# Kernel optimization log

Measured on AMD Instinct MI355X. Metric: run time of the kernel, lower is better.

The kernel has to match this reference:

```python
import jax, jax.numpy as jnp
import numpy as np
import math

B, S, D, H = 8, 1024, 1024, 16
DK = D          # d_k = d_v = d_model (required for the per-head matmul to type-check)
HD = DK // H    # per-head dim = 64


def setup_inputs() -> dict:
    key = jax.random.key(0)
    ks = jax.random.split(key, 10)
    sc = 0.02
    return {
        "source": jax.random.normal(ks[0], (B, S, D), dtype=jnp.float32),
        "target": jax.random.normal(ks[1], (B, S, D), dtype=jnp.float32),
        "wq": jax.random.normal(ks[2], (D, DK), dtype=jnp.float32) * sc,
        "wk": jax.random.normal(ks[3], (D, DK), dtype=jnp.float32) * sc,
        "wv": jax.random.normal(ks[4], (D, DK), dtype=jnp.float32) * sc,
        "WQ": jax.random.normal(ks[5], (H, D, HD), dtype=jnp.float32) * sc,
        "WK": jax.random.normal(ks[6], (H, D, HD), dtype=jnp.float32) * sc,
        "WV": jax.random.normal(ks[7], (H, D, HD), dtype=jnp.float32) * sc,
        "ow": jax.random.normal(ks[8], (DK, D), dtype=jnp.float32) * sc,
        "ob": jnp.zeros((D,), dtype=jnp.float32),
    }


def reference(source, target, wq, wk, wv, WQ, WK, WV, ow, ob):
    # shared projections (nn.Linear, bias=False)
    Q = source @ wq          # (B,S,DK)
    K = target @ wk          # (B,S,DK)
    V = target @ wv          # (B,S,DK)
    # per-head projections Q @ W_Q[i], vectorized over all heads
    q = jnp.einsum('bsk,hkd->bhsd', Q, WQ)   # (B,H,S,HD)
    k = jnp.einsum('bsk,hkd->bhsd', K, WK)
    v = jnp.einsum('bsk,hkd->bhsd', V, WV)
    scores = jnp.einsum('bhqd,bhkd->bhqk', q, k) / math.sqrt(DK)
    # NOTE: original uses nn.Softmax(dim=1) on (B, Sq, Sk) -> normalizes over
    # the QUERY axis; faithful translation => axis=2 of (B,H,Sq,Sk).
    attn = jax.nn.softmax(scores, axis=2)
    o = jnp.einsum('bhqk,bhkd->bhqd', attn, v)          # (B,H,S,HD)
    o = jnp.transpose(o, (0, 2, 1, 3)).reshape(B, S, DK)  # concat heads
    return o @ ow + ob
```

## Files before the change

kernel.cpp:

```cpp
#include <hip/hip_runtime.h>

using u16 = unsigned short;
typedef float f32x4 __attribute__((ext_vector_type(4)));
typedef __bf16 bf16x8 __attribute__((ext_vector_type(8)));
typedef unsigned short u16x4 __attribute__((ext_vector_type(4)));
typedef unsigned short u16x8 __attribute__((ext_vector_type(8)));
typedef unsigned int u32x2 __attribute__((ext_vector_type(2)));

static constexpr float SC2 = 0.03125f * 1.44269504088896f;

static __device__ __forceinline__ u16 f2bf(float f) {
  unsigned u = __builtin_bit_cast(unsigned, f);
  u += 0x7FFFu + ((u >> 16) & 1u);
  return (u16)(u >> 16);
}
static __device__ __forceinline__ float bf2f(u16 h) {
  unsigned u = ((unsigned)h) << 16;
  return __builtin_bit_cast(float, u);
}
static __device__ __forceinline__ unsigned cvt_pk(float lo, float hi) {
  unsigned r;
  asm("v_cvt_pk_bf16_f32 %0, %1, %2" : "=v"(r) : "v"(lo), "v"(hi));
  return r;
}

typedef __attribute__((address_space(3))) unsigned int lds_uint;
typedef __attribute__((address_space(1))) unsigned int g_uint;

static __device__ __forceinline__ void load_lds16(const u16* gp, const void* lp) {
  __builtin_amdgcn_global_load_lds((g_uint*)(unsigned long long)gp,
                                   (lds_uint*)(unsigned int)(unsigned long long)lp,
                                   16, 0, 0);
}

struct Prep {
  const float* src; const float* tgt;
  const float* w[3]; const float* W[3]; const float* ow;
  u16* src_bf; u16* tgt_bf; u16* w_bf[3]; u16* Wt[3]; u16* owT;
};
__global__ __launch_bounds__(256) void k_prep(Prep P) {
  const int bid = blockIdx.x, t = threadIdx.x;
  if (bid < 16384) {
    const float* in = bid < 8192 ? P.src : P.tgt;
    u16* out = bid < 8192 ? P.src_bf : P.tgt_bf;
    int i = (bid & 8191) * 256 + t;
    f32x4 v = reinterpret_cast<const f32x4*>(in)[i];
    u16x4 o;
    o[0] = f2bf(v[0]); o[1] = f2bf(v[1]); o[2] = f2bf(v[2]); o[3] = f2bf(v[3]);
    reinterpret_cast<u16x4*>(out)[i] = o;
  } else if (bid < 19456) {
    int r = bid - 16384;
    int z = r >> 10;
    int i = (r & 1023) * 256 + t;
    f32x4 v = reinterpret_cast<const f32x4*>(P.w[z])[i];
    u16x4 o;
    o[0] = f2bf(v[0]); o[1] = f2bf(v[1]); o[2] = f2bf(v[2]); o[3] = f2bf(v[3]);
    reinterpret_cast<u16x4*>(P.w_bf[z])[i] = o;
  } else if (bid < 31744) {
    int r = bid - 19456;
    int z = r >> 12;
    int idx = (r & 4095) * 256 + t;
    int n = idx >> 10, c = idx & 1023;
    int h = n >> 6, j = n & 63;
    P.Wt[z][idx] = f2bf(P.W[z][(h * 1024 + c) * 64 + j]);
  } else {
    int idx = (bid - 31744) * 256 + t;
    int n = idx >> 10, k = idx & 1023;
    P.owT[idx] = f2bf(P.ow[k * 1024 + n]);
  }
}

struct GemmPtrs { const u16* A; const u16* B; void* C; float scale; int mode; };
struct Gemm3 { GemmPtrs g[3]; };

__global__ __launch_bounds__(256) void k_gemm_bt(Gemm3 P, int N, int K,
                                                 const float* __restrict__ bias) {
  const u16* A  = P.g[blockIdx.z].A;
  const u16* Bt = P.g[blockIdx.z].B;
  const float sc = P.g[blockIdx.z].scale;
  const int mode = P.g[blockIdx.z].mode;
  __shared__ u16 As[2][128 * 64];
  __shared__ u16 Bs[2][128 * 64];
  const int tid = threadIdx.x, lane = tid & 63, w = tid >> 6;
  const int swz = (blockIdx.x & 7) * (gridDim.x >> 3) + (blockIdx.x >> 3);
  const int nbn = N >> 7;
  const int m0 = (swz / nbn) << 7;
  const int n0 = (swz % nbn) << 7;
  const int wr = (w >> 1) << 6, wc = (w & 1) << 6;
  const int l15 = lane & 15, lg = lane >> 4;
  const int srow = tid >> 3;
  const int sslot = (tid & 7) ^ (srow & 7);
  const u16* Ag = A  + (size_t)(m0 + srow) * K + sslot * 8;
  const u16* Bg = Bt + (size_t)(n0 + srow) * K + sslot * 8;

  f32x4 acc[4][4];
#pragma unroll
  for (int i = 0; i < 4; ++i)
#pragma unroll
    for (int j = 0; j < 4; ++j) acc[i][j] = f32x4{0.f, 0.f, 0.f, 0.f};

#pragma unroll
  for (int j = 0; j < 4; ++j) {
    load_lds16(Ag + (size_t)(j * 32) * K, (const char*)As[0] + j * 4096 + tid * 16);
    load_lds16(Bg + (size_t)(j * 32) * K, (const char*)Bs[0] + j * 4096 + tid * 16);
  }
  __syncthreads();

  for (int kt = 0; kt < K; kt += 64) {
    const int buf = (kt >> 6) & 1;
    if (kt + 64 < K) {
#pragma unroll
      for (int j = 0; j < 4; ++j) {
        load_lds16(Ag + (size_t)(j * 32) * K + kt + 64, (const char*)As[buf ^ 1] + j * 4096 + tid * 16);
        load_lds16(Bg + (size_t)(j * 32) * K + kt + 64, (const char*)Bs[buf ^ 1] + j * 4096 + tid * 16);
      }
    }
#pragma unroll
    for (int kh = 0; kh < 2; ++kh) {
      bf16x8 af[4], bfr[4];
#pragma unroll
      for (int i = 0; i < 4; ++i) {
        const int ra = wr + i * 16 + l15;
        const int rb = wc + i * 16 + l15;
        af[i]  = *reinterpret_cast<const bf16x8*>(As[buf] + ra * 64 + ((((kh << 2) | lg) ^ (ra & 7)) << 3));
        bfr[i] = *reinterpret_cast<const bf16x8*>(Bs[buf] + rb * 64 + ((((kh << 2) | lg) ^ (rb & 7)) << 3));
      }
#pragma unroll
      for (int mi = 0; mi < 4; ++mi)
#pragma unroll
        for (int ni = 0; ni < 4; ++ni)
          acc[mi][ni] = __builtin_amdgcn_mfma_f32_16x16x32_bf16(af[mi], bfr[ni], acc[mi][ni], 0, 0, 0);
    }
    __syncthreads();
  }

  const int orow0 = m0 + wr + lg * 4;
  const int ocol0 = n0 + wc + l15;
  if (mode == 1) {
    float* C = (float*)P.g[blockIdx.z].C;
#pragma unroll
    for (int ni = 0; ni < 4; ++ni) {
      float bv = bias ? bias[ocol0 + ni * 16] : 0.f;
#pragma unroll
      for (int mi = 0; mi < 4; ++mi)
#pragma unroll
        for (int r = 0; r < 4; ++r)
          C[(size_t)(orow0 + mi * 16 + r) * N + ocol0 + ni * 16] = acc[mi][ni][r] + bv;
    }
  } else if (mode == 2) {
    u16* C = (u16*)P.g[blockIdx.z].C;
    const int b = m0 >> 10;
    const int kk0 = (orow0 & 1023);
#pragma unroll
    for (int ni = 0; ni < 4; ++ni) {
      const int col = ocol0 + ni * 16;
      const int hh = col >> 6, d = col & 63;
      u16* vbase = C + ((size_t)(b * 16 + hh)) * 65536 + d * 1024 + kk0;
#pragma unroll
      for (int mi = 0; mi < 4; ++mi) {
        u16x4 pv;
#pragma unroll
        for (int r = 0; r < 4; ++r) pv[r] = f2bf(acc[mi][ni][r] * sc);
        *reinterpret_cast<u16x4*>(vbase + mi * 16) = pv;
      }
    }
  } else {
    u16* C = (u16*)P.g[blockIdx.z].C;
#pragma unroll
    for (int ni = 0; ni < 4; ++ni)
#pragma unroll
      for (int mi = 0; mi < 4; ++mi)
#pragma unroll
        for (int r = 0; r < 4; ++r)
          C[(size_t)(orow0 + mi * 16 + r) * N + ocol0 + ni * 16] = f2bf(acc[mi][ni][r] * sc);
  }
}

__global__ __launch_bounds__(256) void k_pass1(const u16* __restrict__ q_all,
                                               const u16* __restrict__ k_all,
                                               float* __restrict__ l_buf) {
  const int bh = blockIdx.x, kb = blockIdx.y;
  const int b = bh >> 4, h = bh & 15;
  __shared__ u16 Qs[2][2048];
  const int t = threadIdx.x;
  const int lane = t & 63, w = t >> 6;
  const int l15 = lane & 15, lg = lane >> 4;
  const u16* qp = q_all + (size_t)b * 1048576 + h * 64;
  const u16* kp = k_all + (size_t)b * 1048576 + h * 64;
  const int kc0 = kb * 128 + w * 32;

  bf16x8 bfr[2][2];
#pragma unroll
  for (int c = 0; c < 2; ++c)
#pragma unroll
    for (int ks = 0; ks < 2; ++ks)
      bfr[c][ks] = *reinterpret_cast<const bf16x8*>(
          kp + (size_t)(kc0 + c * 16 + l15) * 1024 + ks * 32 + lg * 8);

  const int qrow = t >> 3, qslot = (t & 7) ^ (qrow & 7);
  const u16* qg = qp + (size_t)qrow * 1024 + (qslot << 3);

  load_lds16(qg, (const char*)&Qs[0][0] + t * 16);
  __syncthreads();

  float acc0 = 0.f, acc1 = 0.f;
  const int qsw = l15 & 7;

#pragma unroll 1
  for (int qt = 0; qt < 1024; qt += 32) {
    const int buf = (qt >> 5) & 1;
    if (qt + 32 < 1024)
      load_lds16(qg + (size_t)(qt + 32) * 1024, (const char*)&Qs[buf ^ 1][0] + t * 16);
    const u16* Qb = Qs[buf];
    bf16x8 aq[2][2];
#pragma unroll
    for (int qf = 0; qf < 2; ++qf) {
      aq[qf][0] = *reinterpret_cast<const bf16x8*>(Qb + (qf * 16 + l15) * 64 + ((lg ^ qsw) << 3));
      aq[qf][1] = *reinterpret_cast<const bf16x8*>(Qb + (qf * 16 + l15) * 64 + (((4 + lg) ^ qsw) << 3));
    }
#pragma unroll
    for (int qf = 0; qf < 2; ++qf)
#pragma unroll
      for (int c = 0; c < 2; ++c) {
        f32x4 z = {0.f, 0.f, 0.f, 0.f};
        f32x4 s = __builtin_amdgcn_mfma_f32_16x16x32_bf16(aq[qf][0], bfr[c][0], z, 0, 0, 0);
        s = __builtin_amdgcn_mfma_f32_16x16x32_bf16(aq[qf][1], bfr[c][1], s, 0, 0, 0);
        float e = __builtin_amdgcn_exp2f(s[0]) + __builtin_amdgcn_exp2f(s[1])
                + __builtin_amdgcn_exp2f(s[2]) + __builtin_amdgcn_exp2f(s[3]);
        if (c) acc1 += e; else acc0 += e;
      }
    __syncthreads();
  }
  acc0 += __shfl_xor(acc0, 16); acc0 += __shfl_xor(acc0, 32);
  acc1 += __shfl_xor(acc1, 16); acc1 += __shfl_xor(acc1, 32);
  if (lane < 32) {
    int col = kc0 + lane;
    l_buf[(size_t)bh * 1024 + col] = (lane < 16) ? acc0 : acc1;
  }
}

__global__ __launch_bounds__(256, 4) void k_pass2(const u16* __restrict__ q_all,
                                                  const u16* __restrict__ k_all,
                                                  const u16* __restrict__ vT,
                                                  const float* __restrict__ l_buf,
                                                  u16* __restrict__ o_all) {
  const int bh = blockIdx.x, qb = blockIdx.y;
  const int b = bh >> 4, h = bh & 15;
  __shared__ u16 Ks[2][2048];
  __shared__ u16 Vs[2][2048];
  __shared__ u16 p_lds[4][2][640];
  __shared__ float rl_lds[1024];
  const int t = threadIdx.x;
  const int lane = t & 63, w = t >> 6;
  const int l15 = lane & 15, lg = lane >> 4;
  const int q0 = qb * 128 + w * 32;
  const u16* qp = q_all + (size_t)b * 1048576 + h * 64;
  const u16* kp = k_all + (size_t)b * 1048576 + h * 64;
  const u16* vp = vT + (size_t)bh * 65536;

  {
    f32x4 lv = reinterpret_cast<const f32x4*>(l_buf + (size_t)bh * 1024)[t];
    f32x4 rv;
#pragma unroll
    for (int j = 0; j < 4; ++j) rv[j] = 1.0f / lv[j];
    reinterpret_cast<f32x4*>(rl_lds)[t] = rv;
  }

  const int krow = t >> 3, kslot = (t & 7) ^ (krow & 7);
  const u16* kg = kp + (size_t)krow * 1024 + (kslot << 3);
  const int vrow = t >> 2, vslot = (t & 3) ^ (vrow & 3);
  const u16* vg = vp + (size_t)vrow * 1024 + (vslot << 3);

  bf16x8 bq[2][2];
#pragma unroll
  for (int qf = 0; qf < 2; ++qf)
#pragma unroll
    for (int s = 0; s < 2; ++s)
      bq[qf][s] = *reinterpret_cast<const bf16x8*>(
          qp + (size_t)(q0 + qf * 16 + l15) * 1024 + s * 32 + lg * 8);

  f32x4 od[2][4];
#pragma unroll
  for (int qf = 0; qf < 2; ++qf)
#pragma unroll
    for (int n = 0; n < 4; ++n) od[qf][n] = f32x4{0.f, 0.f, 0.f, 0.f};

  load_lds16(kg, (const char*)&Ks[0][0] + t * 16);
  load_lds16(vg, (const char*)&Vs[0][0] + t * 16);
  __syncthreads();

  const int ksw = l15 & 7, vsw = l15 & 3;

#pragma unroll 1
  for (int kt = 0; kt < 1024; kt += 32) {
    const int buf = (kt >> 5) & 1;
    if (kt + 32 < 1024) {
      load_lds16(kg + (size_t)(kt + 32) * 1024, (const char*)&Ks[buf ^ 1][0] + t * 16);
      load_lds16(vg + (kt + 32), (const char*)&Vs[buf ^ 1][0] + t * 16);
    }
    const u16* Kb = Ks[buf];
    const u16* Vb = Vs[buf];
    bf16x8 k00 = *reinterpret_cast<const bf16x8*>(Kb + l15 * 64 + ((lg ^ ksw) << 3));
    bf16x8 k01 = *reinterpret_cast<const bf16x8*>(Kb + l15 * 64 + (((4 + lg) ^ ksw) << 3));
    bf16x8 k10 = *reinterpret_cast<const bf16x8*>(Kb + (16 + l15) * 64 + ((lg ^ ksw) << 3));
    bf16x8 k11 = *reinterpret_cast<const bf16x8*>(Kb + (16 + l15) * 64 + (((4 + lg) ^ ksw) << 3));
    bf16x8 vc[4];
#pragma unroll
    for (int n = 0; n < 4; ++n)
      vc[n] = *reinterpret_cast<const bf16x8*>(Vb + (n * 16 + l15) * 32 + ((lg ^ vsw) << 3));

    f32x4 r0 = *reinterpret_cast<const f32x4*>(&rl_lds[kt + lg * 4]);
    f32x4 r1 = *reinterpret_cast<const f32x4*>(&rl_lds[kt + 16 + lg * 4]);

    u16* pl = p_lds[w][0];
    u16* ph = p_lds[w][1];
#pragma unroll
    for (int qf = 0; qf < 2; ++qf) {
      f32x4 z = {0.f, 0.f, 0.f, 0.f};
      f32x4 s0 = __builtin_amdgcn_mfma_f32_16x16x32_bf16(k00, bq[qf][0], z, 0, 0, 0);
      s0 = __builtin_amdgcn_mfma_f32_16x16x32_bf16(k01, bq[qf][1], s0, 0, 0, 0);
      f32x4 s1 = __builtin_amdgcn_mfma_f32_16x16x32_bf16(k10, bq[qf][0], z, 0, 0, 0);
      s1 = __builtin_amdgcn_mfma_f32_16x16x32_bf16(k11, bq[qf][1], s1, 0, 0, 0);
      u32x2 wlo, whi;
      wlo[0] = cvt_pk(__builtin_amdgcn_exp2f(s0[0]) * r0[0], __builtin_amdgcn_exp2f(s0[1]) * r0[1]);
      wlo[1] = cvt_pk(__builtin_amdgcn_exp2f(s0[2]) * r0[2], __builtin_amdgcn_exp2f(s0[3]) * r0[3]);
      whi[0] = cvt_pk(__builtin_amdgcn_exp2f(s1[0]) * r1[0], __builtin_amdgcn_exp2f(s1[1]) * r1[1]);
      whi[1] = cvt_pk(__builtin_amdgcn_exp2f(s1[2]) * r1[2], __builtin_amdgcn_exp2f(s1[3]) * r1[3]);
      u16* dst = qf ? ph : pl;
      *reinterpret_cast<u32x2*>(dst + l15 * 40 + lg * 4) = wlo;
      *reinterpret_cast<u32x2*>(dst + l15 * 40 + 16 + lg * 4) = whi;
    }
    bf16x8 pa0 = *reinterpret_cast<const bf16x8*>(pl + l15 * 40 + lg * 8);
    bf16x8 pa1 = *reinterpret_cast<const bf16x8*>(ph + l15 * 40 + lg * 8);
#pragma unroll
    for (int n = 0; n < 4; ++n) {
      od[0][n] = __builtin_amdgcn_mfma_f32_16x16x32_bf16(pa0, vc[n], od[0][n], 0, 0, 0);
      od[1][n] = __builtin_amdgcn_mfma_f32_16x16x32_bf16(pa1, vc[n], od[1][n], 0, 0, 0);
    }
    __syncthreads();
  }

  u16* op = o_all + (size_t)b * 1048576 + h * 64;
#pragma unroll
  for (int qf = 0; qf < 2; ++qf)
#pragma unroll
    for (int n = 0; n < 4; ++n)
#pragma unroll
      for (int r = 0; r < 4; ++r)
        op[(size_t)(q0 + qf * 16 + lg * 4 + r) * 1024 + n * 16 + l15] = f2bf(od[qf][n][r]);
}

extern "C" void kernel_launch(void* const* d_in, const int* in_sizes, int n_in,
                              void* d_out, int out_size, void* d_ws, size_t ws_size,
                              hipStream_t stream) {
  (void)in_sizes; (void)n_in; (void)out_size; (void)ws_size;
  char* base = (char*)d_ws;
  size_t off = 0;
  auto alloc = [&](size_t bytes) -> char* {
    char* p = base + off;
    off = (off + bytes + 255) & ~(size_t)255;
    return p;
  };
  u16* src_bf = (u16*)alloc(8ull * 1024 * 1024 * 2);
  u16* tgt_bf = (u16*)alloc(8ull * 1024 * 1024 * 2);
  u16* wq_bf  = (u16*)alloc(1024 * 1024 * 2);
  u16* wk_bf  = (u16*)alloc(1024 * 1024 * 2);
  u16* wv_bf  = (u16*)alloc(1024 * 1024 * 2);
  u16* WQt    = (u16*)alloc(1024 * 1024 * 2);
  u16* WKt    = (u16*)alloc(1024 * 1024 * 2);
  u16* WVt    = (u16*)alloc(1024 * 1024 * 2);
  u16* CqT    = (u16*)alloc(1024 * 1024 * 2);
  u16* CkT    = (u16*)alloc(1024 * 1024 * 2);
  u16* CvT    = (u16*)alloc(1024 * 1024 * 2);
  u16* owT    = (u16*)alloc(1024 * 1024 * 2);
  u16* q_all  = (u16*)alloc(8ull * 1024 * 1024 * 2);
  u16* k_all  = (u16*)alloc(8ull * 1024 * 1024 * 2);
  u16* vT     = (u16*)alloc(8ull * 1024 * 1024 * 2);
  u16* o_all  = (u16*)alloc(8ull * 1024 * 1024 * 2);
  float* l_buf = (float*)alloc(128 * 1024 * 4);

  Prep prep = {
    (const float*)d_in[0], (const float*)d_in[1],
    {(const float*)d_in[2], (const float*)d_in[3], (const float*)d_in[4]},
    {(const float*)d_in[5], (const float*)d_in[6], (const float*)d_in[7]},
    (const float*)d_in[8],
    src_bf, tgt_bf, {wq_bf, wk_bf, wv_bf}, {WQt, WKt, WVt}, owT
  };
  k_prep<<<35840, 256, 0, stream>>>(prep);

  Gemm3 comb = {{{WQt, wq_bf, CqT, SC2, 0}, {WKt, wk_bf, CkT, 1.f, 0}, {WVt, wv_bf, CvT, 1.f, 0}}};
  k_gemm_bt<<<dim3(64, 1, 3), 256, 0, stream>>>(comb, 1024, 1024, nullptr);

  Gemm3 proj = {{{src_bf, CqT, q_all, 1.f, 0}, {tgt_bf, CkT, k_all, 1.f, 0}, {tgt_bf, CvT, vT, 1.f, 2}}};
  k_gemm_bt<<<dim3(512, 1, 3), 256, 0, stream>>>(proj, 1024, 1024, nullptr);

  k_pass1<<<dim3(128, 8), 256, 0, stream>>>(q_all, k_all, l_buf);
  k_pass2<<<dim3(128, 8), 256, 0, stream>>>(q_all, k_all, vT, l_buf, o_all);

  Gemm3 fin = {{{o_all, owT, d_out, 1.f, 1}, {o_all, owT, d_out, 1.f, 1}, {o_all, owT, d_out, 1.f, 1}}};
  k_gemm_bt<<<dim3(512, 1, 1), 256, 0, stream>>>(fin, 1024, 1024, (const float*)d_in[9]);
}
```

Baseline: 215.4 us.

## Fold softmax normalizer into MFMA bias, swizzle attention blocks, widen pass1 Q tiles

The per-column normalizer becomes -log2(l), used as the MFMA accumulator init, so exp2 yields already-normalized probabilities and the per-element multiplies go away. Both attention passes use a 1D grid with a block-index swizzle that changes which blocks run together, aimed at better L2 reuse of K/Q/V. Pass1 now stages 64 query rows per iteration instead of 32, halving loop trips and barriers at the cost of doubled LDS. s_setprio hints are placed around the MFMA sections in pass2.

Result: no change. 212.4 us (-1.4%).

```diff
diff --git a/kernel.cpp b/kernel.cpp
--- a/kernel.cpp
+++ b/kernel.cpp
@@ -179,9 +179,11 @@
 __global__ __launch_bounds__(256) void k_pass1(const u16* __restrict__ q_all,
                                                const u16* __restrict__ k_all,
                                                float* __restrict__ l_buf) {
-  const int bh = blockIdx.x, kb = blockIdx.y;
+  const int bid = blockIdx.x;
+  const int swz = (bid & 7) * 128 + (bid >> 3);
+  const int bh = swz >> 3, kb = swz & 7;
   const int b = bh >> 4, h = bh & 15;
-  __shared__ u16 Qs[2][2048];
+  __shared__ u16 Qs[2][4096];
   const int t = threadIdx.x;
   const int lane = t & 63, w = t >> 6;
   const int l15 = lane & 15, lg = lane >> 4;
@@ -200,35 +202,38 @@
   const int qrow = t >> 3, qslot = (t & 7) ^ (qrow & 7);
   const u16* qg = qp + (size_t)qrow * 1024 + (qslot << 3);
 
-  load_lds16(qg, (const char*)&Qs[0][0] + t * 16);
+#pragma unroll
+  for (int j = 0; j < 2; ++j)
+    load_lds16(qg + (size_t)(j * 32) * 1024, (const char*)&Qs[0][0] + j * 4096 + t * 16);
   __syncthreads();
 
   float acc0 = 0.f, acc1 = 0.f;
   const int qsw = l15 & 7;
 
 #pragma unroll 1
-  for (int qt = 0; qt < 1024; qt += 32) {
-    const int buf = (qt >> 5) & 1;
-    if (qt + 32 < 1024)
-      load_lds16(qg + (size_t)(qt + 32) * 1024, (const char*)&Qs[buf ^ 1][0] + t * 16);
+  for (int qt = 0; qt < 1024; qt += 64) {
+    const int buf = (qt >> 6) & 1;
+    if (qt + 64 < 1024) {
+#pragma unroll
+      for (int j = 0; j < 2; ++j)
+        load_lds16(qg + (size_t)(qt + 64 + j * 32) * 1024,
+                   (const char*)&Qs[buf ^ 1][0] + j * 4096 + t * 16);
+    }
     const u16* Qb = Qs[buf];
-    bf16x8 aq[2][2];
-#pragma unroll
-    for (int qf = 0; qf < 2; ++qf) {
-      aq[qf][0] = *reinterpret_cast<const bf16x8*>(Qb + (qf * 16 + l15) * 64 + ((lg ^ qsw) << 3));
-      aq[qf][1] = *reinterpret_cast<const bf16x8*>(Qb + (qf * 16 + l15) * 64 + (((4 + lg) ^ qsw) << 3));
-    }
-#pragma unroll
-    for (int qf = 0; qf < 2; ++qf)
+#pragma unroll
+    for (int qf = 0; qf < 4; ++qf) {
+      bf16x8 a0 = *reinterpret_cast<const bf16x8*>(Qb + (qf * 16 + l15) * 64 + ((lg ^ qsw) << 3));
+      bf16x8 a1 = *reinterpret_cast<const bf16x8*>(Qb + (qf * 16 + l15) * 64 + (((4 + lg) ^ qsw) << 3));
 #pragma unroll
       for (int c = 0; c < 2; ++c) {
         f32x4 z = {0.f, 0.f, 0.f, 0.f};
-        f32x4 s = __builtin_amdgcn_mfma_f32_16x16x32_bf16(aq[qf][0], bfr[c][0], z, 0, 0, 0);
-        s = __builtin_amdgcn_mfma_f32_16x16x32_bf16(aq[qf][1], bfr[c][1], s, 0, 0, 0);
+        f32x4 s = __builtin_amdgcn_mfma_f32_16x16x32_bf16(a0, bfr[c][0], z, 0, 0, 0);
+        s = __builtin_amdgcn_mfma_f32_16x16x32_bf16(a1, bfr[c][1], s, 0, 0, 0);
         float e = __builtin_amdgcn_exp2f(s[0]) + __builtin_amdgcn_exp2f(s[1])
                 + __builtin_amdgcn_exp2f(s[2]) + __builtin_amdgcn_exp2f(s[3]);
         if (c) acc1 += e; else acc0 += e;
       }
+    }
     __syncthreads();
   }
   acc0 += __shfl_xor(acc0, 16); acc0 += __shfl_xor(acc0, 32);
@@ -244,7 +249,9 @@
                                                   const u16* __restrict__ vT,
                                                   const float* __restrict__ l_buf,
                                                   u16* __restrict__ o_all) {
-  const int bh = blockIdx.x, qb = blockIdx.y;
+  const int bid = blockIdx.x;
+  const int swz = (bid & 7) * 128 + (bid >> 3);
+  const int bh = swz >> 3, qb = swz & 7;
   const int b = bh >> 4, h = bh & 15;
   __shared__ u16 Ks[2][2048];
   __shared__ u16 Vs[2][2048];
@@ -262,7 +269,7 @@
     f32x4 lv = reinterpret_cast<const f32x4*>(l_buf + (size_t)bh * 1024)[t];
     f32x4 rv;
 #pragma unroll
-    for (int j = 0; j < 4; ++j) rv[j] = 1.0f / lv[j];
+    for (int j = 0; j < 4; ++j) rv[j] = -__log2f(lv[j]);
     reinterpret_cast<f32x4*>(rl_lds)[t] = rv;
   }
 
@@ -309,34 +316,37 @@
     for (int n = 0; n < 4; ++n)
       vc[n] = *reinterpret_cast<const bf16x8*>(Vb + (n * 16 + l15) * 32 + ((lg ^ vsw) << 3));
 
-    f32x4 r0 = *reinterpret_cast<const f32x4*>(&rl_lds[kt + lg * 4]);
-    f32x4 r1 = *reinterpret_cast<const f32x4*>(&rl_lds[kt + 16 + lg * 4]);
+    f32x4 b0 = *reinterpret_cast<const f32x4*>(&rl_lds[kt + lg * 4]);
+    f32x4 b1 = *reinterpret_cast<const f32x4*>(&rl_lds[kt + 16 + lg * 4]);
 
     u16* pl = p_lds[w][0];
     u16* ph = p_lds[w][1];
 #pragma unroll
     for (int qf = 0; qf < 2; ++qf) {
-      f32x4 z = {0.f, 0.f, 0.f, 0.f};
-      f32x4 s0 = __builtin_amdgcn_mfma_f32_16x16x32_bf16(k00, bq[qf][0], z, 0, 0, 0);
+      __builtin_amdgcn_s_setprio(1);
+      f32x4 s0 = __builtin_amdgcn_mfma_f32_16x16x32_bf16(k00, bq[qf][0], b0, 0, 0, 0);
       s0 = __builtin_amdgcn_mfma_f32_16x16x32_bf16(k01, bq[qf][1], s0, 0, 0, 0);
-      f32x4 s1 = __builtin_amdgcn_mfma_f32_16x16x32_bf16(k10, bq[qf][0], z, 0, 0, 0);
+      f32x4 s1 = __builtin_amdgcn_mfma_f32_16x16x32_bf16(k10, bq[qf][0], b1, 0, 0, 0);
       s1 = __builtin_amdgcn_mfma_f32_16x16x32_bf16(k11, bq[qf][1], s1, 0, 0, 0);
+      __builtin_amdgcn_s_setprio(0);
       u32x2 wlo, whi;
-      wlo[0] = cvt_pk(__builtin_amdgcn_exp2f(s0[0]) * r0[0], __builtin_amdgcn_exp2f(s0[1]) * r0[1]);
-      wlo[1] = cvt_pk(__builtin_amdgcn_exp2f(s0[2]) * r0[2], __builtin_amdgcn_exp2f(s0[3]) * r0[3]);
-      whi[0] = cvt_pk(__builtin_amdgcn_exp2f(s1[0]) * r1[0], __builtin_amdgcn_exp2f(s1[1]) * r1[1]);
-      whi[1] = cvt_pk(__builtin_amdgcn_exp2f(s1[2]) * r1[2], __builtin_amdgcn_exp2f(s1[3]) * r1[3]);
+      wlo[0] = cvt_pk(__builtin_amdgcn_exp2f(s0[0]), __builtin_amdgcn_exp2f(s0[1]));
+      wlo[1] = cvt_pk(__builtin_amdgcn_exp2f(s0[2]), __builtin_amdgcn_exp2f(s0[3]));
+      whi[0] = cvt_pk(__builtin_amdgcn_exp2f(s1[0]), __builtin_amdgcn_exp2f(s1[1]));
+      whi[1] = cvt_pk(__builtin_amdgcn_exp2f(s1[2]), __builtin_amdgcn_exp2f(s1[3]));
       u16* dst = qf ? ph : pl;
       *reinterpret_cast<u32x2*>(dst + l15 * 40 + lg * 4) = wlo;
       *reinterpret_cast<u32x2*>(dst + l15 * 40 + 16 + lg * 4) = whi;
     }
     bf16x8 pa0 = *reinterpret_cast<const bf16x8*>(pl + l15 * 40 + lg * 8);
     bf16x8 pa1 = *reinterpret_cast<const bf16x8*>(ph + l15 * 40 + lg * 8);
+    __builtin_amdgcn_s_setprio(1);
 #pragma unroll
     for (int n = 0; n < 4; ++n) {
       od[0][n] = __builtin_amdgcn_mfma_f32_16x16x32_bf16(pa0, vc[n], od[0][n], 0, 0, 0);
       od[1][n] = __builtin_amdgcn_mfma_f32_16x16x32_bf16(pa1, vc[n], od[1][n], 0, 0, 0);
     }
+    __builtin_amdgcn_s_setprio(0);
     __syncthreads();
   }
 
@@ -394,8 +404,8 @@
   Gemm3 proj = {{{src_bf, CqT, q_all, 1.f, 0}, {tgt_bf, CkT, k_all, 1.f, 0}, {tgt_bf, CvT, vT, 1.f, 2}}};
   k_gemm_bt<<<dim3(512, 1, 3), 256, 0, stream>>>(proj, 1024, 1024, nullptr);
 
-  k_pass1<<<dim3(128, 8), 256, 0, stream>>>(q_all, k_all, l_buf);
-  k_pass2<<<dim3(128, 8), 256, 0, stream>>>(q_all, k_all, vT, l_buf, o_all);
+  k_pass1<<<1024, 256, 0, stream>>>(q_all, k_all, l_buf);
+  k_pass2<<<1024, 256, 0, stream>>>(q_all, k_all, vT, l_buf, o_all);
 
   Gemm3 fin = {{{o_all, owT, d_out, 1.f, 1}, {o_all, owT, d_out, 1.f, 1}, {o_all, owT, d_out, 1.f, 1}}};
   k_gemm_bt<<<dim3(512, 1, 1), 256, 0, stream>>>(fin, 1024, 1024, (const float*)d_in[9]);
```
